# Performance work log

Measured on AMD Instinct MI355X. Metric: run time of the kernel, lower is better.

Reference implementation:

```python
import jax, jax.numpy as jnp
import numpy as np

N_NODES = 500_000
N_EDGES = 16_000_000
N_COLORS = 64


def _mix(v, c1, c2):
    """32-bit integer hash (lowbias32-style avalanche mix)."""
    v = v.astype(jnp.uint32)
    v = (v ^ (v >> 16)) * jnp.uint32(c1)
    v = (v ^ (v >> 13)) * jnp.uint32(c2)
    return v ^ (v >> 16)


def setup_inputs() -> dict:
    key = jax.random.key(0)
    k1, k2 = jax.random.split(key)
    x = jax.random.randint(k1, (N_NODES,), 0, N_COLORS, dtype=jnp.int32)
    edge_index = jax.random.randint(k2, (2, N_EDGES), 0, N_NODES, dtype=jnp.int32)
    return {"x": x, "edge_index": edge_index}


def reference(x, edge_index):
    """One Weisfeiler-Lehman color-refinement step.

    Faithful semantics of WLConvOptimized.forward: each node's new label is
    determined by the equivalence class of (own label, multiset of incoming
    neighbor labels). Instead of Python tuple-sort + hash()+dict, we use a
    permutation-invariant multiset hash (sum of two independent 32-bit hashes
    of neighbor labels, combined with the node's own label hash) and then a
    sort-based dense relabeling. Nodes get equal output labels iff their
    (label, neighbor-multiset) signatures collide -- same partition as the
    original (up to astronomically unlikely hash collisions); label numbering
    is canonical (sorted-signature order) rather than dict-insertion order.
    """
    num_nodes = x.shape[0]
    row, col = edge_index[0], edge_index[1]  # message flows row (src) -> col (dst)

    # two independent per-label hashes
    ha = _mix(x, 0x045D9F3B, 0x045D9F3B)
    hb = _mix(x, 0x9E3779B1, 0x85EBCA77)

    # permutation-invariant multiset hash of incoming neighbor labels (gather + scatter-add)
    sum_a = jnp.zeros(num_nodes, jnp.uint32).at[col].add(ha[row])
    sum_b = jnp.zeros(num_nodes, jnp.uint32).at[col].add(hb[row])

    # combine own label with neighbor multiset, re-avalanche
    sig_a = _mix(ha * jnp.uint32(0x27D4EB2F) + sum_a, 0xC2B2AE3D, 0x165667B1)
    sig_b = _mix(hb * jnp.uint32(0x61C88647) + sum_b, 0x045D9F3B, 0x27D4EB2F)

    # dense relabel: sort by (sig_a, sig_b), number distinct signatures 0..K-1
    order = jnp.lexsort((sig_b, sig_a))
    sa, sb = sig_a[order], sig_b[order]
    new_grp = jnp.concatenate([
        jnp.zeros(1, jnp.int32),
        ((sa[1:] != sa[:-1]) | (sb[1:] != sb[:-1])).astype(jnp.int32),
    ])
    labels_sorted = jnp.cumsum(new_grp).astype(jnp.int32)
    out = jnp.zeros(num_nodes, jnp.int32).at[order].set(labels_sorted)
    return out
```

## Files before the change

kernel.cpp:

```cpp
#include <hip/hip_runtime.h>
#include <stdint.h>

#define LOG_B 17
#define NB (1u << LOG_B)
#define FINE_NODES 1024
#define NBKT 512
#define CSH 10
#define EPB 16384
#define ITERS (EPB / 4 / 256)

__host__ __device__ constexpr uint32_t cmix(uint32_t v, uint32_t c1, uint32_t c2) {
    v = (v ^ (v >> 16)) * c1;
    v = (v ^ (v >> 13)) * c2;
    return v ^ (v >> 16);
}

__device__ __forceinline__ uint32_t mixh(uint32_t v, uint32_t c1, uint32_t c2) {
    v = (v ^ (v >> 16)) * c1;
    v = (v ^ (v >> 13)) * c2;
    return v ^ (v >> 16);
}

struct Luts { uint32_t ha[64]; uint32_t hb[64]; };
constexpr Luts make_luts() {
    Luts l{};
    for (uint32_t i = 0; i < 64; i++) {
        l.ha[i] = cmix(i, 0x045D9F3Bu, 0x045D9F3Bu);
        l.hb[i] = cmix(i, 0x9E3779B1u, 0x85EBCA77u);
    }
    return l;
}
__constant__ Luts LUT = make_luts();

__global__ __launch_bounds__(256) void k_pre(const int4* __restrict__ x4,
                                             uchar4* __restrict__ xc4, int n4) {
    int i = blockIdx.x * 256 + threadIdx.x;
    if (i >= n4) return;
    int4 v = x4[i];
    xc4[i] = make_uchar4((uint8_t)v.x, (uint8_t)v.y, (uint8_t)v.z, (uint8_t)v.w);
}

__global__ __launch_bounds__(256, 4) void k_bin(const int* __restrict__ row, const int* __restrict__ col,
                                                const uint8_t* __restrict__ xc, uint16_t* __restrict__ bins,
                                                uint32_t* __restrict__ cursor, int E, int cap) {
    __shared__ uint16_t stage[EPB];
    __shared__ uint32_t hist[NBKT];
    __shared__ uint16_t gb16[NBKT];
    __shared__ uint32_t wsum[4];
    int t = threadIdx.x;
    int lane = t & 63, wid = t >> 6;
    int base = blockIdx.x * EPB;
    int nend = min(E - base, EPB);
    for (int b = t; b < NBKT; b += 256) hist[b] = 0;
    __syncthreads();

    const int4* col4 = (const int4*)(col + base);
    const int4* row4 = (const int4*)(row + base);

    bool fast = (nend == EPB);
    uint32_t rec[ITERS * 4];

    if (fast) {
#pragma unroll
        for (int it = 0; it < ITERS; ++it) {
            int k = t + it * 256;
            int4 c = col4[k];
            int4 r = row4[k];
            atomicAdd(&hist[(uint32_t)c.x >> CSH], 1u);
            atomicAdd(&hist[(uint32_t)c.y >> CSH], 1u);
            atomicAdd(&hist[(uint32_t)c.z >> CSH], 1u);
            atomicAdd(&hist[(uint32_t)c.w >> CSH], 1u);
            rec[it * 4 + 0] = ((uint32_t)c.x << 6) | (uint32_t)xc[r.x];
            rec[it * 4 + 1] = ((uint32_t)c.y << 6) | (uint32_t)xc[r.y];
            rec[it * 4 + 2] = ((uint32_t)c.z << 6) | (uint32_t)xc[r.z];
            rec[it * 4 + 3] = ((uint32_t)c.w << 6) | (uint32_t)xc[r.w];
        }
    } else {
        int n4 = nend >> 2;
        for (int k = t; k < n4; k += 256) {
            int4 c = col4[k];
            atomicAdd(&hist[(uint32_t)c.x >> CSH], 1u);
            atomicAdd(&hist[(uint32_t)c.y >> CSH], 1u);
            atomicAdd(&hist[(uint32_t)c.z >> CSH], 1u);
            atomicAdd(&hist[(uint32_t)c.w >> CSH], 1u);
        }
        for (int k = (n4 << 2) + t; k < nend; k += 256)
            atomicAdd(&hist[(uint32_t)col[base + k] >> CSH], 1u);
    }
    __syncthreads();

    int b0 = 2 * t;
    uint32_t h0 = hist[b0], h1 = hist[b0 + 1];
    uint32_t s = h0 + h1;
    uint32_t inc = s;
    for (int off = 1; off < 64; off <<= 1) {
        uint32_t nv = __shfl_up(inc, (unsigned)off, 64);
        if (lane >= off) inc += nv;
    }
    if (lane == 63) wsum[wid] = inc;
    __syncthreads();
    uint32_t woff = 0;
    for (int w = 0; w < wid; w++) woff += wsum[w];
    uint32_t e0 = woff + inc - s;
    uint32_t g0 = h0 ? atomicAdd(&cursor[b0], h0) : 0u;
    uint32_t g1 = h1 ? atomicAdd(&cursor[b0 + 1], h1) : 0u;
    gb16[b0] = (uint16_t)g0;
    gb16[b0 + 1] = (uint16_t)g1;
    hist[b0] = e0 << 16;
    hist[b0 + 1] = (e0 + h0) << 16;
    __syncthreads();

    if (fast) {
#pragma unroll
        for (int it = 0; it < ITERS * 4; ++it) {
            uint32_t rv = rec[it];
            uint32_t b = rv >> 16;
            uint32_t o = atomicAdd(&hist[b], 1u);
            stage[(o >> 16) + (o & 0xFFFFu)] = (uint16_t)rv;
        }
    } else {
        int n4 = nend >> 2;
        for (int k = t; k < n4; k += 256) {
            int4 c = col4[k];
            int4 r = row4[k];
            {
                uint32_t d = (uint32_t)c.x, b = d >> CSH;
                uint32_t o = atomicAdd(&hist[b], 1u);
                stage[(o >> 16) + (o & 0xFFFFu)] = (uint16_t)(((d & 1023u) << 6) | (uint32_t)xc[r.x]);
            }
            {
                uint32_t d = (uint32_t)c.y, b = d >> CSH;
                uint32_t o = atomicAdd(&hist[b], 1u);
                stage[(o >> 16) + (o & 0xFFFFu)] = (uint16_t)(((d & 1023u) << 6) | (uint32_t)xc[r.y]);
            }
            {
                uint32_t d = (uint32_t)c.z, b = d >> CSH;
                uint32_t o = atomicAdd(&hist[b], 1u);
                stage[(o >> 16) + (o & 0xFFFFu)] = (uint16_t)(((d & 1023u) << 6) | (uint32_t)xc[r.z]);
            }
            {
                uint32_t d = (uint32_t)c.w, b = d >> CSH;
                uint32_t o = atomicAdd(&hist[b], 1u);
                stage[(o >> 16) + (o & 0xFFFFu)] = (uint16_t)(((d & 1023u) << 6) | (uint32_t)xc[r.w]);
            }
        }
        for (int k = (n4 << 2) + t; k < nend; k += 256) {
            int i = base + k;
            uint32_t d = (uint32_t)col[i], b = d >> CSH;
            uint32_t o = atomicAdd(&hist[b], 1u);
            stage[(o >> 16) + (o & 0xFFFFu)] = (uint16_t)(((d & 1023u) << 6) | (uint32_t)xc[row[i]]);
        }
    }
    __syncthreads();

    int sub = lane >> 4, l16 = lane & 15;
    for (int b = wid * 4 + sub; b < NBKT; b += 16) {
        uint32_t hv = hist[b];
        uint32_t cnt = hv & 0xFFFFu;
        if (!cnt) continue;
        uint32_t s0 = hv >> 16;
        uint16_t* dst = bins + (size_t)b * (uint32_t)cap + gb16[b];
        for (uint32_t off = l16; off < cnt; off += 16)
            dst[off] = stage[s0 + off];
    }
}

__global__ __launch_bounds__(512) void k_accsig(const uint16_t* __restrict__ bins,
                                                const uint32_t* __restrict__ cursor,
                                                const uint8_t* __restrict__ xc,
                                                unsigned long long* __restrict__ sigs,
                                                uint32_t* __restrict__ bcnt, int N, int cap) {
    __shared__ uint32_t cnt[FINE_NODES * 16];
    int t = threadIdx.x;
    int b = blockIdx.x;
    for (int i = t; i < FINE_NODES * 16; i += 512) cnt[i] = 0;
    __syncthreads();
    uint32_t m = cursor[b];
    const uint16_t* mybins = bins + (size_t)b * (uint32_t)cap;
    const uint2* p16v = (const uint2*)mybins;
    uint32_t m4 = m >> 2;
    for (uint32_t k = t; k < m4; k += 512) {
        uint2 rv = p16v[k];
        {
            uint32_t rec = rv.x & 0xFFFFu, n = rec >> 6, c = rec & 63u;
            atomicAdd(&cnt[n * 16 + (c >> 2)], 1u << (8u * (c & 3u)));
        }
        {
            uint32_t rec = rv.x >> 16, n = rec >> 6, c = rec & 63u;
            atomicAdd(&cnt[n * 16 + (c >> 2)], 1u << (8u * (c & 3u)));
        }
        {
            uint32_t rec = rv.y & 0xFFFFu, n = rec >> 6, c = rec & 63u;
            atomicAdd(&cnt[n * 16 + (c >> 2)], 1u << (8u * (c & 3u)));
        }
        {
            uint32_t rec = rv.y >> 16, n = rec >> 6, c = rec & 63u;
            atomicAdd(&cnt[n * 16 + (c >> 2)], 1u << (8u * (c & 3u)));
        }
    }
    for (uint32_t k = (m4 << 2) + t; k < m; k += 512) {
        uint32_t rec = mybins[k], n = rec >> 6, c = rec & 63u;
        atomicAdd(&cnt[n * 16 + (c >> 2)], 1u << (8u * (c & 3u)));
    }
    __syncthreads();

    for (int n = t; n < FINE_NODES; n += 512) {
        int g = b * FINE_NODES + n;
        if (g >= N) break;
        uint32_t sum_a = 0, sum_b = 0;
#pragma unroll
        for (int w = 0; w < 16; w++) {
            uint32_t wp = (uint32_t)(w + n) & 15u;
            uint32_t v = cnt[n * 16 + wp];
            uint32_t c0 = v & 255u, c1 = (v >> 8) & 255u, c2 = (v >> 16) & 255u, c3 = v >> 24;
            sum_a += c0 * LUT.ha[4 * wp] + c1 * LUT.ha[4 * wp + 1]
                   + c2 * LUT.ha[4 * wp + 2] + c3 * LUT.ha[4 * wp + 3];
            sum_b += c0 * LUT.hb[4 * wp] + c1 * LUT.hb[4 * wp + 1]
                   + c2 * LUT.hb[4 * wp + 2] + c3 * LUT.hb[4 * wp + 3];
        }
        uint32_t xv = (uint32_t)xc[g];
        uint32_t ha = LUT.ha[xv];
        uint32_t hb = LUT.hb[xv];
        uint32_t sa = mixh(ha * 0x27D4EB2Fu + sum_a, 0xC2B2AE3Du, 0x165667B1u);
        uint32_t sb = mixh(hb * 0x61C88647u + sum_b, 0x045D9F3Bu, 0x27D4EB2Fu);
        unsigned long long key = ((unsigned long long)sa << 32) | (unsigned long long)sb;
        sigs[g] = key;
        atomicAdd(&bcnt[(uint32_t)(key >> (64 - LOG_B))], 1u);
    }
}

__global__ __launch_bounds__(256) void k_scan1(const uint32_t* __restrict__ in,
                                               uint32_t* __restrict__ out,
                                               uint32_t* __restrict__ part) {
    __shared__ uint32_t wsum[4];
    int t = threadIdx.x;
    int lane = t & 63, wid = t >> 6;
    int base = blockIdx.x * 1024 + 4 * t;
    uint4 v = *(const uint4*)(in + base);
    uint32_t s = v.x + v.y + v.z + v.w;
    uint32_t inc = s;
    for (int off = 1; off < 64; off <<= 1) {
        uint32_t nv = __shfl_up(inc, (unsigned)off, 64);
        if (lane >= off) inc += nv;
    }
    if (lane == 63) wsum[wid] = inc;
    __syncthreads();
    uint32_t woff = 0;
    for (int w = 0; w < wid; w++) woff += wsum[w];
    uint32_t e = woff + inc - s;
    uint4 o;
    o.x = e; o.y = e + v.x; o.z = o.y + v.y; o.w = o.z + v.z;
    *(uint4*)(out + base) = o;
    if (t == 255) part[blockIdx.x] = wsum[0] + wsum[1] + wsum[2] + wsum[3];
}

__global__ void k_scan2(uint32_t* __restrict__ part) {
    __shared__ uint32_t s[256];
    int t = threadIdx.x;
    uint32_t v = part[t];
    s[t] = v;
    __syncthreads();
    for (int off = 1; off < 256; off <<= 1) {
        uint32_t add = (t >= off) ? s[t - off] : 0u;
        __syncthreads();
        s[t] += add;
        __syncthreads();
    }
    part[t] = s[t] - v;
}

__global__ __launch_bounds__(256) void k_scan3(uint32_t* __restrict__ out,
                                               const uint32_t* __restrict__ part) {
    int base = blockIdx.x * 1024 + 4 * threadIdx.x;
    uint32_t p = part[blockIdx.x];
    uint4 v = *(const uint4*)(out + base);
    v.x += p; v.y += p; v.z += p; v.w += p;
    *(uint4*)(out + base) = v;
}

__global__ void k_scatter(const unsigned long long* __restrict__ sigs,
                          const uint32_t* __restrict__ boff, uint32_t* __restrict__ bcur,
                          unsigned long long* __restrict__ skey, uint32_t* __restrict__ snode,
                          int N) {
    int i = blockIdx.x * blockDim.x + threadIdx.x;
    if (i >= N) return;
    unsigned long long key = sigs[i];
    uint32_t b = (uint32_t)(key >> (64 - LOG_B));
    uint32_t pos = boff[b] + atomicAdd(&bcur[b], 1u);
    skey[pos] = key;
    snode[pos] = (uint32_t)i;
}

__global__ void k_bsort(unsigned long long* __restrict__ skey, uint32_t* __restrict__ snode,
                        const uint32_t* __restrict__ boff, uint32_t* __restrict__ ldx,
                        uint32_t* __restrict__ dcnt, int N) {
    int b = blockIdx.x * blockDim.x + threadIdx.x;
    if (b >= (int)NB) return;
    uint32_t s0 = boff[b];
    uint32_t s1 = (b == (int)NB - 1) ? (uint32_t)N : boff[b + 1];
    for (uint32_t i = s0 + 1; i < s1; i++) {
        unsigned long long k = skey[i];
        uint32_t nd = snode[i];
        uint32_t j = i;
        while (j > s0 && skey[j - 1] > k) {
            skey[j] = skey[j - 1];
            snode[j] = snode[j - 1];
            j--;
        }
        skey[j] = k;
        snode[j] = nd;
    }
    uint32_t d = 0;
    unsigned long long prev = 0ull;
    for (uint32_t i = s0; i < s1; i++) {
        unsigned long long k = skey[i];
        if (i == s0 || k != prev) d++;
        prev = k;
        ldx[i] = d - 1;
    }
    dcnt[b] = d;
}

__global__ void k_out(const unsigned long long* __restrict__ skey,
                      const uint32_t* __restrict__ snode, const uint32_t* __restrict__ ldx,
                      const uint32_t* __restrict__ doff, int* __restrict__ out, int N) {
    int i = blockIdx.x * blockDim.x + threadIdx.x;
    if (i >= N) return;
    unsigned long long key = skey[i];
    uint32_t b = (uint32_t)(key >> (64 - LOG_B));
    out[snode[i]] = (int)(doff[b] + ldx[i]);
}

extern "C" void kernel_launch(void* const* d_in, const int* in_sizes, int n_in,
                              void* d_out, int out_size, void* d_ws, size_t ws_size,
                              hipStream_t stream) {
    const int* x = (const int*)d_in[0];
    const int* ei = (const int*)d_in[1];
    int N = in_sizes[0];
    int E = in_sizes[1] / 2;
    const int* row = ei;
    const int* col = ei + E;

    int nacc = (N + FINE_NODES - 1) / FINE_NODES;
    int cap = E / NBKT + (E / NBKT) / 16 + 1024;
    cap = (cap + 3) & ~3;

    char* p = (char*)d_ws;
    auto alloc = [&](size_t bytes) -> char* {
        char* r = p;
        p += (bytes + 255) & ~(size_t)255;
        return r;
    };
    uint32_t* cursor = (uint32_t*)alloc((size_t)NBKT * 4);
    uint32_t* bcnt   = (uint32_t*)alloc((size_t)NB * 4);
    uint32_t* bcur   = (uint32_t*)alloc((size_t)NB * 4);
    uint32_t* dcnt   = (uint32_t*)alloc((size_t)NB * 4);
    uint32_t* part   = (uint32_t*)alloc(256 * 4);
    size_t zbytes = (size_t)(p - (char*)d_ws);
    uint8_t* xc = (uint8_t*)alloc((size_t)N);
    unsigned long long* sigs = (unsigned long long*)alloc((size_t)N * 8);
    uint16_t* bins = (uint16_t*)alloc((size_t)NBKT * cap * 2);
    char* q = (char*)bins;
    auto alias = [&](size_t bytes) -> char* {
        char* r = q;
        q += (bytes + 255) & ~(size_t)255;
        return r;
    };
    unsigned long long* skey = (unsigned long long*)alias((size_t)N * 8);
    uint32_t* snode = (uint32_t*)alias((size_t)N * 4);
    uint32_t* ldx   = (uint32_t*)alias((size_t)N * 4);
    uint32_t* boff  = (uint32_t*)alias((size_t)NB * 4);
    uint32_t* doff  = (uint32_t*)alias((size_t)NB * 4);

    hipMemsetAsync(d_ws, 0, zbytes, stream);

    int nbN = (N + 255) / 256;
    int nbBin = (E + EPB - 1) / EPB;
    int n4 = N / 4;

    k_pre<<<(n4 + 255) / 256, 256, 0, stream>>>((const int4*)x, (uchar4*)xc, n4);
    k_bin<<<nbBin, 256, 0, stream>>>(row, col, xc, bins, cursor, E, cap);
    k_accsig<<<nacc, 512, 0, stream>>>(bins, cursor, xc, sigs, bcnt, N, cap);

    k_scan1<<<NB / 1024, 256, 0, stream>>>(bcnt, boff, part);
    k_scan2<<<1, 256, 0, stream>>>(part);
    k_scan3<<<NB / 1024, 256, 0, stream>>>(boff, part);

    k_scatter<<<nbN, 256, 0, stream>>>(sigs, boff, bcur, skey, snode, N);
    k_bsort<<<NB / 256, 256, 0, stream>>>(skey, snode, boff, ldx, dcnt, N);

    k_scan1<<<NB / 1024, 256, 0, stream>>>(dcnt, doff, part);
    k_scan2<<<1, 256, 0, stream>>>(part);
    k_scan3<<<NB / 1024, 256, 0, stream>>>(doff, part);

    k_out<<<nbN, 256, 0, stream>>>(skey, snode, ldx, doff, (int*)d_out, N);
}
```

Baseline: 398.9 us.

## Accumulate neighbor hash sums directly in LDS instead of packed color counts

The accumulation kernel drops its per-node 64-color packed 8-bit count histogram (64KB LDS) and instead atomically adds the per-color hash values into two per-node 32-bit sums held in LDS, with the LUT staged in shared memory. This removes the 16-word reduction pass per node and shrinks LDS from 64KB to 8KB, allowing 1024-thread blocks. In exchange each edge now issues two LDS atomics instead of one, contending on only 1024 addresses per block. It also removes the implicit 255-per-color count limit of the packed histogram.

```diff
diff --git a/kernel.cpp b/kernel.cpp
--- a/kernel.cpp
+++ b/kernel.cpp
@@ -165,64 +165,62 @@
     }
 }
 
-__global__ __launch_bounds__(512) void k_accsig(const uint16_t* __restrict__ bins,
-                                                const uint32_t* __restrict__ cursor,
-                                                const uint8_t* __restrict__ xc,
-                                                unsigned long long* __restrict__ sigs,
-                                                uint32_t* __restrict__ bcnt, int N, int cap) {
-    __shared__ uint32_t cnt[FINE_NODES * 16];
+__global__ __launch_bounds__(1024) void k_accsig(const uint16_t* __restrict__ bins,
+                                                 const uint32_t* __restrict__ cursor,
+                                                 const uint8_t* __restrict__ xc,
+                                                 unsigned long long* __restrict__ sigs,
+                                                 uint32_t* __restrict__ bcnt, int N, int cap) {
+    __shared__ uint32_t sA[FINE_NODES];
+    __shared__ uint32_t sB[FINE_NODES];
+    __shared__ uint32_t lA[64], lB[64];
     int t = threadIdx.x;
     int b = blockIdx.x;
-    for (int i = t; i < FINE_NODES * 16; i += 512) cnt[i] = 0;
-    __syncthreads();
+    sA[t] = 0;
+    sB[t] = 0;
+    if (t < 64) { lA[t] = LUT.ha[t]; lB[t] = LUT.hb[t]; }
+    __syncthreads();
+
     uint32_t m = cursor[b];
     const uint16_t* mybins = bins + (size_t)b * (uint32_t)cap;
     const uint2* p16v = (const uint2*)mybins;
     uint32_t m4 = m >> 2;
-    for (uint32_t k = t; k < m4; k += 512) {
+    for (uint32_t k = t; k < m4; k += 1024) {
         uint2 rv = p16v[k];
         {
             uint32_t rec = rv.x & 0xFFFFu, n = rec >> 6, c = rec & 63u;
-            atomicAdd(&cnt[n * 16 + (c >> 2)], 1u << (8u * (c & 3u)));
+            atomicAdd(&sA[n], lA[c]);
+            atomicAdd(&sB[n], lB[c]);
         }
         {
             uint32_t rec = rv.x >> 16, n = rec >> 6, c = rec & 63u;
-            atomicAdd(&cnt[n * 16 + (c >> 2)], 1u << (8u * (c & 3u)));
+            atomicAdd(&sA[n], lA[c]);
+            atomicAdd(&sB[n], lB[c]);
         }
         {
             uint32_t rec = rv.y & 0xFFFFu, n = rec >> 6, c = rec & 63u;
-            atomicAdd(&cnt[n * 16 + (c >> 2)], 1u << (8u * (c & 3u)));
+            atomicAdd(&sA[n], lA[c]);
+            atomicAdd(&sB[n], lB[c]);
         }
         {
             uint32_t rec = rv.y >> 16, n = rec >> 6, c = rec & 63u;
-            atomicAdd(&cnt[n * 16 + (c >> 2)], 1u << (8u * (c & 3u)));
-        }
-    }
-    for (uint32_t k = (m4 << 2) + t; k < m; k += 512) {
+            atomicAdd(&sA[n], lA[c]);
+            atomicAdd(&sB[n], lB[c]);
+        }
+    }
+    for (uint32_t k = (m4 << 2) + t; k < m; k += 1024) {
         uint32_t rec = mybins[k], n = rec >> 6, c = rec & 63u;
-        atomicAdd(&cnt[n * 16 + (c >> 2)], 1u << (8u * (c & 3u)));
-    }
-    __syncthreads();
-
-    for (int n = t; n < FINE_NODES; n += 512) {
-        int g = b * FINE_NODES + n;
-        if (g >= N) break;
-        uint32_t sum_a = 0, sum_b = 0;
-#pragma unroll
-        for (int w = 0; w < 16; w++) {
-            uint32_t wp = (uint32_t)(w + n) & 15u;
-            uint32_t v = cnt[n * 16 + wp];
-            uint32_t c0 = v & 255u, c1 = (v >> 8) & 255u, c2 = (v >> 16) & 255u, c3 = v >> 24;
-            sum_a += c0 * LUT.ha[4 * wp] + c1 * LUT.ha[4 * wp + 1]
-                   + c2 * LUT.ha[4 * wp + 2] + c3 * LUT.ha[4 * wp + 3];
-            sum_b += c0 * LUT.hb[4 * wp] + c1 * LUT.hb[4 * wp + 1]
-                   + c2 * LUT.hb[4 * wp + 2] + c3 * LUT.hb[4 * wp + 3];
-        }
+        atomicAdd(&sA[n], lA[c]);
+        atomicAdd(&sB[n], lB[c]);
+    }
+    __syncthreads();
+
+    int g = b * FINE_NODES + t;
+    if (g < N) {
         uint32_t xv = (uint32_t)xc[g];
-        uint32_t ha = LUT.ha[xv];
-        uint32_t hb = LUT.hb[xv];
-        uint32_t sa = mixh(ha * 0x27D4EB2Fu + sum_a, 0xC2B2AE3Du, 0x165667B1u);
-        uint32_t sb = mixh(hb * 0x61C88647u + sum_b, 0x045D9F3Bu, 0x27D4EB2Fu);
+        uint32_t ha = lA[xv];
+        uint32_t hb = lB[xv];
+        uint32_t sa = mixh(ha * 0x27D4EB2Fu + sA[t], 0xC2B2AE3Du, 0x165667B1u);
+        uint32_t sb = mixh(hb * 0x61C88647u + sB[t], 0x045D9F3Bu, 0x27D4EB2Fu);
         unsigned long long key = ((unsigned long long)sa << 32) | (unsigned long long)sb;
         sigs[g] = key;
         atomicAdd(&bcnt[(uint32_t)(key >> (64 - LOG_B))], 1u);
@@ -380,7 +378,7 @@
 
     k_pre<<<(n4 + 255) / 256, 256, 0, stream>>>((const int4*)x, (uchar4*)xc, n4);
     k_bin<<<nbBin, 256, 0, stream>>>(row, col, xc, bins, cursor, E, cap);
-    k_accsig<<<nacc, 512, 0, stream>>>(bins, cursor, xc, sigs, bcnt, N, cap);
+    k_accsig<<<nacc, 1024, 0, stream>>>(bins, cursor, xc, sigs, bcnt, N, cap);
 
     k_scan1<<<NB / 1024, 256, 0, stream>>>(bcnt, boff, part);
     k_scan2<<<1, 256, 0, stream>>>(part);
```

Measured after the change: 397.9 us. No clear change (-0.2%).
